# Performance work log

Hardware: AMD Instinct MI355X
Metric: run time of the kernel (lower is better)

Reference implementation:

```python
import jax, jax.numpy as jnp
import numpy as np

N_NODES = 50000
N_EDGES = 800000
EPS = 1e-5
NEG_SLOPE = 0.2


def _gatv2(x, src, dst, Wl, bl, Wr, br, att, bias, concat, N):
    # PyG GATv2Conv: xl = lin_l(x) (source side), xr = lin_r(x) (target side)
    H, C = att.shape
    xl = (x @ Wl + bl).reshape(N, H, C)
    xr = (x @ Wr + br).reshape(N, H, C)
    # per-edge message: leaky_relu(xl[j] + xr[i]), attention logit = <att, .>
    z = xl[src] + xr[dst]                      # [E, H, C]
    z = jnp.where(z > 0, z, NEG_SLOPE * z)
    logits = jnp.einsum('ehc,hc->eh', z, att)  # [E, H]
    # segment softmax over incoming edges of each target node
    m = jax.lax.stop_gradient(jax.ops.segment_max(logits, dst, num_segments=N))
    p = jnp.exp(logits - m[dst])
    s = jax.ops.segment_sum(p, dst, num_segments=N)
    alpha = p / s[dst]                         # [E, H]
    out = jax.ops.segment_sum(xl[src] * alpha[..., None], dst, num_segments=N)  # [N, H, C]
    out = out.reshape(N, H * C) if concat else out.mean(axis=1)
    return out + bias


def _bn(x, g, b):
    mu = x.mean(axis=0)
    v = x.var(axis=0)
    return (x - mu) * jax.lax.rsqrt(v + EPS) * g + b


def setup_inputs() -> dict:
    key = jax.random.key(0)
    ks = jax.random.split(key, 16)
    x = jax.random.normal(ks[0], (N_NODES, 2), jnp.float32)
    edge_index = jax.random.randint(ks[1], (2, N_EDGES), 0, N_NODES, dtype=jnp.int64)

    def lin(k, i, o):
        return jax.random.normal(k, (i, o), jnp.float32) * (1.0 / np.sqrt(i))

    inp = {'x': x, 'edge_index': edge_index}
    # layer 1: in=2, heads=8, out=16, concat
    inp['W1l'] = lin(ks[2], 2, 128); inp['b1l'] = jnp.zeros((128,), jnp.float32)
    inp['W1r'] = lin(ks[3], 2, 128); inp['b1r'] = jnp.zeros((128,), jnp.float32)
    inp['a1'] = jax.random.normal(ks[4], (8, 16), jnp.float32) * 0.1
    inp['bias1'] = jnp.zeros((128,), jnp.float32)
    inp['g1'] = jnp.ones((128,), jnp.float32); inp['be1'] = jnp.zeros((128,), jnp.float32)
    # layer 2: in=128, heads=4, out=16, concat
    inp['W2l'] = lin(ks[5], 128, 64); inp['b2l'] = jnp.zeros((64,), jnp.float32)
    inp['W2r'] = lin(ks[6], 128, 64); inp['b2r'] = jnp.zeros((64,), jnp.float32)
    inp['a2'] = jax.random.normal(ks[7], (4, 16), jnp.float32) * 0.1
    inp['bias2'] = jnp.zeros((64,), jnp.float32)
    inp['g2'] = jnp.ones((64,), jnp.float32); inp['be2'] = jnp.zeros((64,), jnp.float32)
    # layer 3: in=64, heads=1, out=2, mean (concat=False)
    inp['W3l'] = lin(ks[8], 64, 2); inp['b3l'] = jnp.zeros((2,), jnp.float32)
    inp['W3r'] = lin(ks[9], 64, 2); inp['b3r'] = jnp.zeros((2,), jnp.float32)
    inp['a3'] = jax.random.normal(ks[10], (1, 2), jnp.float32) * 0.1
    inp['bias3'] = jnp.zeros((2,), jnp.float32)
    return inp


def reference(x, edge_index, W1l, b1l, W1r, b1r, a1, bias1, g1, be1,
              W2l, b2l, W2r, b2r, a2, bias2, g2, be2,
              W3l, b3l, W3r, b3r, a3, bias3):
    N = x.shape[0]
    loops = jnp.arange(N, dtype=edge_index.dtype)
    src = jnp.concatenate([edge_index[0], loops])  # add self loops (PyG default)
    dst = jnp.concatenate([edge_index[1], loops])
    h = _gatv2(x, src, dst, W1l, b1l, W1r, b1r, a1, bias1, True, N)
    h = jax.nn.elu(_bn(h, g1, be1))  # dropout is identity in eval
    h = _gatv2(h, src, dst, W2l, b2l, W2r, b2r, a2, bias2, True, N)
    h = jax.nn.elu(_bn(h, g2, be2))
    return _gatv2(h, src, dst, W3l, b3l, W3r, b3r, a3, bias3, False, N)
```

## Files before the change

### kernel.cpp

```cpp
#include <hip/hip_runtime.h>
#include <hip/hip_bf16.h>

#define N_NODES 50000
#define N_E0    800000
#define N_ET    850000
#define EPSBN   1e-5f
#define LOG2E   1.4426950408889634f

#define LEAKY(z) fmaxf((z), 0.2f * (z))

#define OFF_C 0
#define OFF_A (128*N_NODES)
#define OFF_B (192*N_NODES)
#define OFF_STATS (256*N_NODES)
#define OFF_S1R (OFF_STATS + 512)
#define OFF_S2R (OFF_S1R + 16384)
#define OFF_P (OFF_S2R + 8192)
#define N_PARAM_TOT 118312
#define OFF_ROWPTR (OFF_P + N_PARAM_TOT)
#define OFF_DEG    (OFF_ROWPTR + 50001)
#define OFF_CURSOR (OFF_DEG + 50000)
#define OFF_BSUM   (OFF_CURSOR + 50000)
#define OFF_COL    (OFF_BSUM + 256)
#define OFF_FLAGS  (OFF_COL + 850064)
#define OFF_SCNT   (OFF_FLAGS + 2)

#define BK_CAP 131072
#define BK_CHUNK 2048

__device__ __forceinline__ float bf2f(unsigned short u) {
    return __uint_as_float(((unsigned int)u) << 16);
}
__device__ __forceinline__ unsigned short f2bf(float f) {
    unsigned int u = __float_as_uint(f);
    u += 0x7FFFu + ((u >> 16) & 1u);
    return (unsigned short)(u >> 16);
}

__global__ void prep_kernel(const unsigned short* xr, const int* ei, int* flags,
                            int* deg, float* stats, float* s1r, float* s2r, int* scnt) {
    int i = blockIdx.x * 256 + threadIdx.x;
    if (i < N_NODES) deg[i] = 0;
    if (i < 512) stats[i] = 0.f;
    if (i < 16384) s1r[i] = 0.f;
    if (i < 8192)  s2r[i] = 0.f;
    if (i < 8) scnt[i] = 0;
    if (blockIdx.x == 0) {
        __shared__ int c1, c2;
        if (threadIdx.x == 0) { c1 = 0; c2 = 0; }
        __syncthreads();
        int t = threadIdx.x;
        int l1 = 0, l2 = 0;
        for (int k = t; k < 2048; k += 256) {
            float v = bf2f(xr[k]);
            if (!(fabsf(v) <= 100.0f)) l1++;
            if (ei[2 * k + 1] != 0) l2++;
        }
        atomicAdd(&c1, l1);
        atomicAdd(&c2, l2);
        __syncthreads();
        if (t == 0) {
            flags[0] = (c1 > 16) ? 1 : 0;
            flags[1] = (c2 == 0) ? 1 : 0;
        }
    }
}

struct ParamPtrs { const void* p[23]; };

__global__ void convert_kernel(ParamPtrs ps, float* dst, const int* flags) {
    const int sizes[23] = {100000, 256,128,256,128,128,128,128,128,
                           8192,64,8192,64,64,64,64,64,
                           128,2,128,2,2,2};
    int g = blockIdx.x * 256 + threadIdx.x;
    if (g >= N_PARAM_TOT) return;
    int t = 0, off = g;
    while (off >= sizes[t]) { off -= sizes[t]; t++; }
    float v;
    if (flags[0]) v = ((const float*)ps.p[t])[off];
    else          v = bf2f(((const unsigned short*)ps.p[t])[off]);
    if (t == 5 || t == 13 || t == 21) v *= LOG2E;
    dst[g] = v;
}

__global__ void bucket_kernel(const int* ei, const int* flags, int* scnt,
                              int* dstb, int* srcb) {
    __shared__ int lcnt[8];
    __shared__ int lbase[8];
    int tid = threadIdx.x;
    if (tid < 8) lcnt[tid] = 0;
    __syncthreads();
    int base_e = blockIdx.x * BK_CHUNK;
    int i64 = flags[1];
    int src[8], dst[8], pos[8];
    #pragma unroll
    for (int u = 0; u < 8; u++) {
        int e = base_e + u * 256 + tid;
        if (e < N_ET) {
            int s, d;
            if (e < N_E0) {
                d = i64 ? ei[2 * (N_E0 + e)] : ei[N_E0 + e];
                s = i64 ? ei[2 * e] : ei[e];
            } else { s = d = e - N_E0; }
            src[u] = s; dst[u] = d;
            pos[u] = atomicAdd(&lcnt[d / 6250], 1);
        } else dst[u] = -1;
    }
    __syncthreads();
    if (tid < 8) lbase[tid] = atomicAdd(&scnt[tid], lcnt[tid]);
    __syncthreads();
    #pragma unroll
    for (int u = 0; u < 8; u++) {
        if (dst[u] >= 0) {
            int st = dst[u] / 6250;
            int gp = st * BK_CAP + lbase[st] + pos[u];
            dstb[gp] = dst[u];
            srcb[gp] = src[u];
        }
    }
}

__global__ void hist2_kernel(const int* scnt, const int* dstb, int* deg) {
    int stripe = blockIdx.x & 7;
    int bi = blockIdx.x >> 3;
    int cnt = scnt[stripe];
    const int* db = dstb + stripe * BK_CAP;
    for (int t = bi * 256 + threadIdx.x; t < cnt; t += 32 * 256)
        atomicAdd(&deg[db[t]], 1);
}

__global__ void scan1_kernel(const int* deg, int* row_ptr, int* bsum) {
    __shared__ int sh[256];
    int i = blockIdx.x * 256 + threadIdx.x;
    int v = (i < N_NODES) ? deg[i] : 0;
    sh[threadIdx.x] = v;
    __syncthreads();
    for (int off = 1; off < 256; off <<= 1) {
        int t = (threadIdx.x >= off) ? sh[threadIdx.x - off] : 0;
        __syncthreads();
        sh[threadIdx.x] += t;
        __syncthreads();
    }
    if (i < N_NODES) row_ptr[i] = sh[threadIdx.x] - v;
    if (threadIdx.x == 255) bsum[blockIdx.x] = sh[255];
}

__global__ void scan23_kernel(int* row_ptr, int* cursor, const int* bsum) {
    __shared__ int sh[256];
    int t = threadIdx.x;
    int v = (t < 196) ? bsum[t] : 0;
    sh[t] = v;
    __syncthreads();
    for (int off = 1; off < 256; off <<= 1) {
        int u = (t >= off) ? sh[t - off] : 0;
        __syncthreads();
        sh[t] += u;
        __syncthreads();
    }
    int prefix = (blockIdx.x == 0) ? 0 : sh[blockIdx.x - 1];
    int i = blockIdx.x * 256 + t;
    if (i < N_NODES) {
        int r = row_ptr[i] + prefix;
        row_ptr[i] = r;
        cursor[i] = r;
    }
    if (i == 0) row_ptr[N_NODES] = N_ET;
}

__global__ void scatter2_kernel(const int* scnt, const int* dstb, const int* srcb,
                                int* cursor, int* col) {
    int stripe = blockIdx.x & 7;
    int bi = blockIdx.x >> 3;
    int cnt = scnt[stripe];
    int off = stripe * BK_CAP;
    for (int t = bi * 256 + threadIdx.x; t < cnt; t += 32 * 256) {
        int d = dstb[off + t];
        int pos = atomicAdd(&cursor[d], 1);
        col[pos] = srcb[off + t];
    }
}

__global__ void __launch_bounds__(256) gather1_kernel(
    const int* row_ptr, const int* col, const float* x,
    const float* W1l, const float* b1l, const float* W1r, const float* b1r,
    const float* att, const float* bias, unsigned int* Cb, float* s1r)
{
    int gid = blockIdx.x * 256 + threadIdx.x;
    int n = gid >> 6;
    int lane = threadIdx.x & 63;
    float2 wl0 = *(const float2*)(W1l + 2 * lane);
    float2 wl1 = *(const float2*)(W1l + 128 + 2 * lane);
    float2 bl  = *(const float2*)(b1l + 2 * lane);
    float2 wr0 = *(const float2*)(W1r + 2 * lane);
    float2 wr1 = *(const float2*)(W1r + 128 + 2 * lane);
    float2 br  = *(const float2*)(b1r + 2 * lane);
    float2 at  = *(const float2*)(att + 2 * lane);
    float2 xd  = *(const float2*)(x + 2 * n);
    float xr0 = fmaf(xd.x, wr0.x, fmaf(xd.y, wr1.x, br.x));
    float xr1 = fmaf(xd.x, wr0.y, fmaf(xd.y, wr1.y, br.y));
    int base = __builtin_amdgcn_readfirstlane(row_ptr[n]);
    int deg  = __builtin_amdgcn_readfirstlane(row_ptr[n + 1]) - base;
    float acc0 = 0.f, acc1 = 0.f, den = 0.f;
    for (int j0 = 0; j0 < deg; j0 += 64) {
        int cnt = deg - j0; if (cnt > 64) cnt = 64;
        int msrc = col[base + j0 + lane];
        int j = 0;
        for (; j + 8 <= cnt; j += 8) {
            int s[8];
            #pragma unroll
            for (int u = 0; u < 8; u++) s[u] = __builtin_amdgcn_readlane(msrc, j + u);
            float2 xs[8];
            #pragma unroll
            for (int u = 0; u < 8; u++) xs[u] = *(const float2*)(x + 2 * s[u]);
            float xl0[8], xl1[8], part[8];
            #pragma unroll
            for (int u = 0; u < 8; u++) {
                xl0[u] = fmaf(xs[u].x, wl0.x, fmaf(xs[u].y, wl1.x, bl.x));
                xl1[u] = fmaf(xs[u].x, wl0.y, fmaf(xs[u].y, wl1.y, bl.y));
                float z0 = LEAKY(xl0[u] + xr0);
                float z1 = LEAKY(xl1[u] + xr1);
                part[u] = fmaf(z0, at.x, z1 * at.y);
            }
            #pragma unroll
            for (int m = 1; m <= 4; m <<= 1) {
                #pragma unroll
                for (int u = 0; u < 8; u++) part[u] += __shfl_xor(part[u], m, 64);
            }
            #pragma unroll
            for (int u = 0; u < 8; u++) {
                float p = exp2f(part[u]);
                acc0 = fmaf(p, xl0[u], acc0);
                acc1 = fmaf(p, xl1[u], acc1);
                den += p;
            }
        }
        for (; j < cnt; ++j) {
            int s0 = __builtin_amdgcn_readlane(msrc, j);
            float2 xs = *(const float2*)(x + 2 * s0);
            float xl0s = fmaf(xs.x, wl0.x, fmaf(xs.y, wl1.x, bl.x));
            float xl1s = fmaf(xs.x, wl0.y, fmaf(xs.y, wl1.y, bl.y));
            float z0 = LEAKY(xl0s + xr0);
            float z1 = LEAKY(xl1s + xr1);
            float part = fmaf(z0, at.x, z1 * at.y);
            part += __shfl_xor(part, 1, 64);
            part += __shfl_xor(part, 2, 64);
            part += __shfl_xor(part, 4, 64);
            float p = exp2f(part);
            acc0 = fmaf(p, xl0s, acc0);
            acc1 = fmaf(p, xl1s, acc1);
            den += p;
        }
    }
    float inv = 1.f / den;
    float2 bi = *(const float2*)(bias + 2 * lane);
    float2 outv;
    outv.x = fmaf(acc0, inv, bi.x);
    outv.y = fmaf(acc1, inv, bi.y);
    Cb[n * 64 + lane] = ((unsigned int)f2bf(outv.y) << 16) | f2bf(outv.x);
    __shared__ float sred[4][128];
    __shared__ float qred[4][128];
    int wv = threadIdx.x >> 6;
    sred[wv][2 * lane]     = outv.x;
    sred[wv][2 * lane + 1] = outv.y;
    qred[wv][2 * lane]     = outv.x * outv.x;
    qred[wv][2 * lane + 1] = outv.y * outv.y;
    __syncthreads();
    int t = threadIdx.x;
    float a;
    if (t < 128) a = sred[0][t] + sred[1][t] + sred[2][t] + sred[3][t];
    else { int c = t - 128; a = qred[0][c] + qred[1][c] + qred[2][c] + qred[3][c]; }
    atomicAdd(&s1r[(blockIdx.x & 63) * 256 + t], a);
}

__global__ void red1_kernel(const float* s1r, float* stats) {
    int t = threadIdx.x;
    int r0 = blockIdx.x * 8;
    float a = 0.f;
    #pragma unroll
    for (int r = 0; r < 8; r++) a += s1r[(r0 + r) * 256 + t];
    atomicAdd(&stats[t], a);
}

__global__ void __launch_bounds__(256) lin2_kernel(
    const unsigned int* Cb, const float* stats, const float* g1, const float* be1,
    const float* Wl, const float* bl, const float* Wr, const float* br,
    unsigned short* xl2b, float* xr2)
{
    __shared__ float h[64 * 132];
    int tid = threadIdx.x;
    int nb = blockIdx.x * 64;
    for (int i = tid; i < 64 * 64; i += 256) {
        int ni = i >> 6, kp = i & 63;
        int n = nb + ni;
        int k = 2 * kp;
        float v0 = 0.f, v1 = 0.f;
        if (n < N_NODES) {
            unsigned int pk = Cb[n * 64 + kp];
            float val0 = __uint_as_float(pk << 16);
            float val1 = __uint_as_float(pk & 0xffff0000u);
            float mu0 = stats[k] * (1.0f / N_NODES);
            float var0 = stats[128 + k] * (1.0f / N_NODES) - mu0 * mu0;
            float sc0 = g1[k] * rsqrtf(var0 + EPSBN);
            float b0 = (val0 - mu0) * sc0 + be1[k];
            v0 = b0 > 0.f ? b0 : __expf(b0) - 1.f;
            float mu1 = stats[k + 1] * (1.0f / N_NODES);
            float var1 = stats[128 + k + 1] * (1.0f / N_NODES) - mu1 * mu1;
            float sc1 = g1[k + 1] * rsqrtf(var1 + EPSBN);
            float b1 = (val1 - mu1) * sc1 + be1[k + 1];
            v1 = b1 > 0.f ? b1 : __expf(b1) - 1.f;
        }
        h[ni * 132 + k]     = v0;
        h[ni * 132 + k + 1] = v1;
    }
    __syncthreads();
    int kt = (tid & 15) * 4;
    int nt = (tid >> 4) * 4;
    float accl[4][4], accr[4][4];
    #pragma unroll
    for (int i = 0; i < 4; i++) {
        #pragma unroll
        for (int k = 0; k < 4; k++) { accl[i][k] = 0.f; accr[i][k] = 0.f; }
    }
    for (int j = 0; j < 128; j += 4) {
        float4 hv[4];
        #pragma unroll
        for (int i = 0; i < 4; i++)
            hv[i] = *(const float4*)&h[(nt + i) * 132 + j];
        #pragma unroll
        for (int jj = 0; jj < 4; jj++) {
            float4 wl4 = *(const float4*)&Wl[(j + jj) * 64 + kt];
            float4 wr4 = *(const float4*)&Wr[(j + jj) * 64 + kt];
            #pragma unroll
            for (int i = 0; i < 4; i++) {
                float hvv = (jj == 0) ? hv[i].x : (jj == 1) ? hv[i].y :
                            (jj == 2) ? hv[i].z : hv[i].w;
                accl[i][0] += hvv * wl4.x; accl[i][1] += hvv * wl4.y;
                accl[i][2] += hvv * wl4.z; accl[i][3] += hvv * wl4.w;
                accr[i][0] += hvv * wr4.x; accr[i][1] += hvv * wr4.y;
                accr[i][2] += hvv * wr4.z; accr[i][3] += hvv * wr4.w;
            }
        }
    }
    float4 blv = *(const float4*)&bl[kt];
    float4 brv = *(const float4*)&br[kt];
    #pragma unroll
    for (int i = 0; i < 4; i++) {
        int n = nb + nt + i;
        if (n < N_NODES) {
            ushort4 ob;
            ob.x = f2bf(accl[i][0] + blv.x);
            ob.y = f2bf(accl[i][1] + blv.y);
            ob.z = f2bf(accl[i][2] + blv.z);
            ob.w = f2bf(accl[i][3] + blv.w);
            *(ushort4*)&xl2b[n * 64 + kt] = ob;
            float4 o;
            o.x = accr[i][0] + brv.x; o.y = accr[i][1] + brv.y;
            o.z = accr[i][2] + brv.z; o.w = accr[i][3] + brv.w;
            *(float4*)&xr2[n * 64 + kt] = o;
        }
    }
}

__global__ void __launch_bounds__(256) gather2_kernel(
    const int* row_ptr, const int* col, const unsigned short* xl2b, const float* xr2,
    const float* att, const float* bias, float* C, float* s2r)
{
    int gid = blockIdx.x * 256 + threadIdx.x;
    int n = gid >> 6;
    int lane = threadIdx.x & 63;
    int grp = lane >> 4;
    int cidx = lane & 15;
    float4 xrv = *(const float4*)(xr2 + n * 64 + 4 * cidx);
    float4 atv = *(const float4*)(att + 4 * cidx);
    int base = __builtin_amdgcn_readfirstlane(row_ptr[n]);
    int deg  = __builtin_amdgcn_readfirstlane(row_ptr[n + 1]) - base;
    float4 acc = make_float4(0.f, 0.f, 0.f, 0.f);
    float den = 0.f;
    for (int j0 = 0; j0 < deg; j0 += 64) {
        int cnt = deg - j0; if (cnt > 64) cnt = 64;
        int msrc = col[base + j0 + lane];
        for (int j4 = 0; j4 < cnt; j4 += 8) {
            int e0 = j4 + grp, e1 = j4 + 4 + grp;
            int s0 = __shfl(msrc, e0, 64);
            int s1 = __shfl(msrc, e1, 64);
            bool v0 = e0 < cnt, v1 = e1 < cnt;
            s0 = v0 ? s0 : 0;
            s1 = v1 ? s1 : 0;
            uint2 ba = *(const uint2*)(xl2b + (size_t)s0 * 64 + 4 * cidx);
            uint2 bb = *(const uint2*)(xl2b + (size_t)s1 * 64 + 4 * cidx);
            float a0 = __uint_as_float(ba.x << 16);
            float a1 = __uint_as_float(ba.x & 0xffff0000u);
            float a2 = __uint_as_float(ba.y << 16);
            float a3 = __uint_as_float(ba.y & 0xffff0000u);
            float b0 = __uint_as_float(bb.x << 16);
            float b1 = __uint_as_float(bb.x & 0xffff0000u);
            float b2 = __uint_as_float(bb.y << 16);
            float b3 = __uint_as_float(bb.y & 0xffff0000u);
            float pa = LEAKY(a0 + xrv.x) * atv.x;
            pa = fmaf(LEAKY(a1 + xrv.y), atv.y, pa);
            pa = fmaf(LEAKY(a2 + xrv.z), atv.z, pa);
            pa = fmaf(LEAKY(a3 + xrv.w), atv.w, pa);
            float pb = LEAKY(b0 + xrv.x) * atv.x;
            pb = fmaf(LEAKY(b1 + xrv.y), atv.y, pb);
            pb = fmaf(LEAKY(b2 + xrv.z), atv.z, pb);
            pb = fmaf(LEAKY(b3 + xrv.w), atv.w, pb);
            pa += __shfl_xor(pa, 1, 64);
            pa += __shfl_xor(pa, 2, 64);
            pb += __shfl_xor(pb, 1, 64);
            pb += __shfl_xor(pb, 2, 64);
            float ea = v0 ? exp2f(pa) : 0.f;
            float eb = v1 ? exp2f(pb) : 0.f;
            acc.x = fmaf(ea, a0, acc.x); acc.x = fmaf(eb, b0, acc.x);
            acc.y = fmaf(ea, a1, acc.y); acc.y = fmaf(eb, b1, acc.y);
            acc.z = fmaf(ea, a2, acc.z); acc.z = fmaf(eb, b2, acc.z);
            acc.w = fmaf(ea, a3, acc.w); acc.w = fmaf(eb, b3, acc.w);
            den += ea + eb;
        }
    }
    acc.x += __shfl_xor(acc.x, 16, 64); acc.x += __shfl_xor(acc.x, 32, 64);
    acc.y += __shfl_xor(acc.y, 16, 64); acc.y += __shfl_xor(acc.y, 32, 64);
    acc.z += __shfl_xor(acc.z, 16, 64); acc.z += __shfl_xor(acc.z, 32, 64);
    acc.w += __shfl_xor(acc.w, 16, 64); acc.w += __shfl_xor(acc.w, 32, 64);
    den += __shfl_xor(den, 16, 64);
    den += __shfl_xor(den, 32, 64);
    float inv = 1.f / den;
    float4 bi = *(const float4*)(bias + 4 * cidx);
    float4 o;
    o.x = fmaf(acc.x, inv, bi.x);
    o.y = fmaf(acc.y, inv, bi.y);
    o.z = fmaf(acc.z, inv, bi.z);
    o.w = fmaf(acc.w, inv, bi.w);
    if (lane < 16) *(float4*)(C + n * 64 + 4 * cidx) = o;
    __shared__ float sred[4][64];
    __shared__ float qred[4][64];
    int wv = threadIdx.x >> 6;
    if (lane < 16) {
        int c = 4 * cidx;
        sred[wv][c]     = o.x; qred[wv][c]     = o.x * o.x;
        sred[wv][c + 1] = o.y; qred[wv][c + 1] = o.y * o.y;
        sred[wv][c + 2] = o.z; qred[wv][c + 2] = o.z * o.z;
        sred[wv][c + 3] = o.w; qred[wv][c + 3] = o.w * o.w;
    }
    __syncthreads();
    int t = threadIdx.x;
    if (t < 128) {
        float a;
        if (t < 64) a = sred[0][t] + sred[1][t] + sred[2][t] + sred[3][t];
        else { int c = t - 64; a = qred[0][c] + qred[1][c] + qred[2][c] + qred[3][c]; }
        atomicAdd(&s2r[(blockIdx.x & 63) * 128 + t], a);
    }
}

__global__ void red2_kernel(const float* s2r, float* stats) {
    int t = threadIdx.x;
    int r0 = blockIdx.x * 8;
    float a = 0.f;
    #pragma unroll
    for (int r = 0; r < 8; r++) a += s2r[(r0 + r) * 128 + t];
    atomicAdd(&stats[t], a);
}

__global__ void __launch_bounds__(256) lin3_kernel(
    const float* C, const float* stats2, const float* g2, const float* be2,
    const float* Wl, const float* bl, const float* Wr, const float* br,
    float* xl3, float* xr3)
{
    int gid = blockIdx.x * 256 + threadIdx.x;
    int n = gid >> 6;
    int lane = threadIdx.x & 63;
    if (n >= N_NODES) return;
    float mu = stats2[lane] * (1.0f / N_NODES);
    float var = stats2[64 + lane] * (1.0f / N_NODES) - mu * mu;
    float sc = g2[lane] * rsqrtf(var + EPSBN);
    float of = be2[lane] - mu * sc;
    float v = C[n * 64 + lane] * sc + of;
    float h = v > 0.f ? v : __expf(v) - 1.f;
    float2 wlv = *(const float2*)(Wl + 2 * lane);
    float2 wrv = *(const float2*)(Wr + 2 * lane);
    float a0 = h * wlv.x, a1 = h * wlv.y;
    float r0 = h * wrv.x, r1 = h * wrv.y;
    #pragma unroll
    for (int m = 1; m < 64; m <<= 1) {
        a0 += __shfl_xor(a0, m, 64);
        a1 += __shfl_xor(a1, m, 64);
        r0 += __shfl_xor(r0, m, 64);
        r1 += __shfl_xor(r1, m, 64);
    }
    if (lane == 0) {
        xl3[2 * n]     = a0 + bl[0];
        xl3[2 * n + 1] = a1 + bl[1];
        xr3[2 * n]     = r0 + br[0];
        xr3[2 * n + 1] = r1 + br[1];
    }
}

__global__ void __launch_bounds__(256) gather3_kernel(
    const int* row_ptr, const int* col,
    const float* xl3, const float* xr3,
    const float* att, const float* bias,
    void* out, const int* flags) {
    int gid = blockIdx.x * 256 + threadIdx.x;
    int n = gid >> 2;
    int q = threadIdx.x & 3;
    if (n >= N_NODES) return;
    float a0 = att[0], a1 = att[1];
    float xr0 = xr3[2 * n], xr1 = xr3[2 * n + 1];
    float acc0 = 0.f, acc1 = 0.f, den = 0.f;
    int e0 = row_ptr[n], e1 = row_ptr[n + 1];
    for (int e = e0 + q; e < e1; e += 4) {
        int src = col[e];
        float2 xs = *(const float2*)(xl3 + 2 * src);
        float z0 = LEAKY(xs.x + xr0);
        float z1 = LEAKY(xs.y + xr1);
        float p = exp2f(fmaf(z0, a0, z1 * a1));
        acc0 = fmaf(p, xs.x, acc0);
        acc1 = fmaf(p, xs.y, acc1);
        den += p;
    }
    acc0 += __shfl_xor(acc0, 1, 64); acc0 += __shfl_xor(acc0, 2, 64);
    acc1 += __shfl_xor(acc1, 1, 64); acc1 += __shfl_xor(acc1, 2, 64);
    den  += __shfl_xor(den, 1, 64);  den  += __shfl_xor(den, 2, 64);
    if (q == 0) {
        float inv = 1.f / den;
        float v0 = fmaf(acc0, inv, bias[0]);
        float v1 = fmaf(acc1, inv, bias[1]);
        if (flags[0]) {
            ((float*)out)[2 * n] = v0;
            ((float*)out)[2 * n + 1] = v1;
        } else {
            ((__hip_bfloat16*)out)[2 * n] = __float2bfloat16(v0);
            ((__hip_bfloat16*)out)[2 * n + 1] = __float2bfloat16(v1);
        }
    }
}

extern "C" void kernel_launch(void* const* d_in, const int* in_sizes, int n_in,
                              void* d_out, int out_size, void* d_ws, size_t ws_size,
                              hipStream_t stream) {
    float* W = (float*)d_ws;
    float* C = W + OFF_C;
    float* A = W + OFF_A;
    float* B = W + OFF_B;
    float* STATS = W + OFF_STATS;
    float* S1R = W + OFF_S1R;
    float* S2R = W + OFF_S2R;
    float* P = W + OFF_P;
    int* ROWPTR = (int*)(W + OFF_ROWPTR);
    int* DEG    = (int*)(W + OFF_DEG);
    int* CURSOR = (int*)(W + OFF_CURSOR);
    int* BSUM   = (int*)(W + OFF_BSUM);
    int* COL    = (int*)(W + OFF_COL);
    int* FLAGS  = (int*)(W + OFF_FLAGS);
    int* SCNT   = (int*)(W + OFF_SCNT);
    int* DSTB   = (int*)(W + OFF_C);
    int* SRCB   = DSTB + 8 * BK_CAP;

    const int* ei = (const int*)d_in[1];

    float* Px  = P;
    float* W1l = Px + 100000; float* b1l = W1l + 256; float* W1r = b1l + 128; float* b1r = W1r + 256;
    float* a1  = b1r + 128;   float* bias1 = a1 + 128; float* g1 = bias1 + 128; float* be1 = g1 + 128;
    float* W2l = be1 + 128;   float* b2l = W2l + 8192; float* W2r = b2l + 64;  float* b2r = W2r + 8192;
    float* a2  = b2r + 64;    float* bias2 = a2 + 64;  float* g2 = bias2 + 64; float* be2 = g2 + 64;
    float* W3l = be2 + 64;    float* b3l = W3l + 128;  float* W3r = b3l + 2;   float* b3r = W3r + 128;
    float* a3  = b3r + 2;     float* bias3 = a3 + 2;

    prep_kernel<<<196, 256, 0, stream>>>((const unsigned short*)d_in[0], ei, FLAGS, DEG, STATS, S1R, S2R, SCNT);

    ParamPtrs ps;
    ps.p[0] = d_in[0];
    for (int j = 1; j < 23; j++) ps.p[j] = d_in[j + 1];
    convert_kernel<<<(N_PARAM_TOT + 255) / 256, 256, 0, stream>>>(ps, P, FLAGS);

    bucket_kernel<<<(N_ET + BK_CHUNK - 1) / BK_CHUNK, 256, 0, stream>>>(ei, FLAGS, SCNT, DSTB, SRCB);
    hist2_kernel<<<256, 256, 0, stream>>>(SCNT, DSTB, DEG);
    scan1_kernel<<<196, 256, 0, stream>>>(DEG, ROWPTR, BSUM);
    scan23_kernel<<<196, 256, 0, stream>>>(ROWPTR, CURSOR, BSUM);
    scatter2_kernel<<<256, 256, 0, stream>>>(SCNT, DSTB, SRCB, CURSOR, COL);

    gather1_kernel<<<N_NODES * 64 / 256, 256, 0, stream>>>(ROWPTR, COL, Px, W1l, b1l, W1r, b1r, a1, bias1, (unsigned int*)C, S1R);
    red1_kernel<<<8, 256, 0, stream>>>(S1R, STATS);

    lin2_kernel<<<(N_NODES + 63) / 64, 256, 0, stream>>>((const unsigned int*)C, STATS, g1, be1, W2l, b2l, W2r, b2r, (unsigned short*)A, B);
    gather2_kernel<<<N_NODES * 64 / 256, 256, 0, stream>>>(ROWPTR, COL, (const unsigned short*)A, B, a2, bias2, C, S2R);
    red2_kernel<<<8, 128, 0, stream>>>(S2R, STATS + 256);

    lin3_kernel<<<N_NODES * 64 / 256, 256, 0, stream>>>(C, STATS + 256, g2, be2, W3l, b3l, W3r, b3r, A, B);
    gather3_kernel<<<(N_NODES * 4 + 255) / 256, 256, 0, stream>>>(ROWPTR, COL, A, B, a3, bias3, d_out, FLAGS);
}
```

Baseline: 338.9 us.

## Split layer-1 gather wavefront into two half-waves processing alternate edges

The layer-1 GATv2 gather kernel now has each lane handle 4 channels instead of 2. The two 32-lane halves of a wavefront process alternate edges in parallel and are combined with a cross-half shuffle at the end. This halves the serial edge iterations per node and shortens the per-edge head reduction from three shuffles to two. In exchange each lane does twice the arithmetic per edge, padded edges are masked with a valid predicate, and an extra final reduction is added.

```diff
diff --git a/kernel.cpp b/kernel.cpp
--- a/kernel.cpp
+++ b/kernel.cpp
@@ -188,82 +188,84 @@
     int gid = blockIdx.x * 256 + threadIdx.x;
     int n = gid >> 6;
     int lane = threadIdx.x & 63;
-    float2 wl0 = *(const float2*)(W1l + 2 * lane);
-    float2 wl1 = *(const float2*)(W1l + 128 + 2 * lane);
-    float2 bl  = *(const float2*)(b1l + 2 * lane);
-    float2 wr0 = *(const float2*)(W1r + 2 * lane);
-    float2 wr1 = *(const float2*)(W1r + 128 + 2 * lane);
-    float2 br  = *(const float2*)(b1r + 2 * lane);
-    float2 at  = *(const float2*)(att + 2 * lane);
+    int g = lane >> 5;
+    int cl = lane & 31;
+    int cb = cl * 4;
+    float4 wl0 = *(const float4*)(W1l + cb);
+    float4 wl1 = *(const float4*)(W1l + 128 + cb);
+    float4 blv = *(const float4*)(b1l + cb);
+    float4 atv = *(const float4*)(att + cb);
     float2 xd  = *(const float2*)(x + 2 * n);
-    float xr0 = fmaf(xd.x, wr0.x, fmaf(xd.y, wr1.x, br.x));
-    float xr1 = fmaf(xd.x, wr0.y, fmaf(xd.y, wr1.y, br.y));
+    float4 wr0 = *(const float4*)(W1r + cb);
+    float4 wr1 = *(const float4*)(W1r + 128 + cb);
+    float4 brv = *(const float4*)(b1r + cb);
+    float4 xrk;
+    xrk.x = fmaf(xd.x, wr0.x, fmaf(xd.y, wr1.x, brv.x));
+    xrk.y = fmaf(xd.x, wr0.y, fmaf(xd.y, wr1.y, brv.y));
+    xrk.z = fmaf(xd.x, wr0.z, fmaf(xd.y, wr1.z, brv.z));
+    xrk.w = fmaf(xd.x, wr0.w, fmaf(xd.y, wr1.w, brv.w));
     int base = __builtin_amdgcn_readfirstlane(row_ptr[n]);
     int deg  = __builtin_amdgcn_readfirstlane(row_ptr[n + 1]) - base;
-    float acc0 = 0.f, acc1 = 0.f, den = 0.f;
+    float4 acc = make_float4(0.f, 0.f, 0.f, 0.f);
+    float den = 0.f;
     for (int j0 = 0; j0 < deg; j0 += 64) {
         int cnt = deg - j0; if (cnt > 64) cnt = 64;
         int msrc = col[base + j0 + lane];
-        int j = 0;
-        for (; j + 8 <= cnt; j += 8) {
-            int s[8];
+        for (int j2 = 0; j2 < cnt; j2 += 8) {
             #pragma unroll
-            for (int u = 0; u < 8; u++) s[u] = __builtin_amdgcn_readlane(msrc, j + u);
-            float2 xs[8];
-            #pragma unroll
-            for (int u = 0; u < 8; u++) xs[u] = *(const float2*)(x + 2 * s[u]);
-            float xl0[8], xl1[8], part[8];
-            #pragma unroll
-            for (int u = 0; u < 8; u++) {
-                xl0[u] = fmaf(xs[u].x, wl0.x, fmaf(xs[u].y, wl1.x, bl.x));
-                xl1[u] = fmaf(xs[u].x, wl0.y, fmaf(xs[u].y, wl1.y, bl.y));
-                float z0 = LEAKY(xl0[u] + xr0);
-                float z1 = LEAKY(xl1[u] + xr1);
-                part[u] = fmaf(z0, at.x, z1 * at.y);
-            }
-            #pragma unroll
-            for (int m = 1; m <= 4; m <<= 1) {
-                #pragma unroll
-                for (int u = 0; u < 8; u++) part[u] += __shfl_xor(part[u], m, 64);
-            }
-            #pragma unroll
-            for (int u = 0; u < 8; u++) {
-                float p = exp2f(part[u]);
-                acc0 = fmaf(p, xl0[u], acc0);
-                acc1 = fmaf(p, xl1[u], acc1);
+            for (int u = 0; u < 4; u++) {
+                int e = j2 + 2 * u + g;
+                int s = __shfl(msrc, e, 64);
+                bool valid = e < cnt;
+                s = valid ? s : 0;
+                float2 xs = *(const float2*)(x + 2 * s);
+                float4 xl;
+                xl.x = fmaf(xs.x, wl0.x, fmaf(xs.y, wl1.x, blv.x));
+                xl.y = fmaf(xs.x, wl0.y, fmaf(xs.y, wl1.y, blv.y));
+                xl.z = fmaf(xs.x, wl0.z, fmaf(xs.y, wl1.z, blv.z));
+                xl.w = fmaf(xs.x, wl0.w, fmaf(xs.y, wl1.w, blv.w));
+                float part = LEAKY(xl.x + xrk.x) * atv.x;
+                part = fmaf(LEAKY(xl.y + xrk.y), atv.y, part);
+                part = fmaf(LEAKY(xl.z + xrk.z), atv.z, part);
+                part = fmaf(LEAKY(xl.w + xrk.w), atv.w, part);
+                part += __shfl_xor(part, 1, 64);
+                part += __shfl_xor(part, 2, 64);
+                float p = valid ? exp2f(part) : 0.f;
+                acc.x = fmaf(p, xl.x, acc.x);
+                acc.y = fmaf(p, xl.y, acc.y);
+                acc.z = fmaf(p, xl.z, acc.z);
+                acc.w = fmaf(p, xl.w, acc.w);
                 den += p;
             }
         }
-        for (; j < cnt; ++j) {
-            int s0 = __builtin_amdgcn_readlane(msrc, j);
-            float2 xs = *(const float2*)(x + 2 * s0);
-            float xl0s = fmaf(xs.x, wl0.x, fmaf(xs.y, wl1.x, bl.x));
-            float xl1s = fmaf(xs.x, wl0.y, fmaf(xs.y, wl1.y, bl.y));
-            float z0 = LEAKY(xl0s + xr0);
-            float z1 = LEAKY(xl1s + xr1);
-            float part = fmaf(z0, at.x, z1 * at.y);
-            part += __shfl_xor(part, 1, 64);
-            part += __shfl_xor(part, 2, 64);
-            part += __shfl_xor(part, 4, 64);
-            float p = exp2f(part);
-            acc0 = fmaf(p, xl0s, acc0);
-            acc1 = fmaf(p, xl1s, acc1);
-            den += p;
-        }
-    }
+    }
+    acc.x += __shfl_xor(acc.x, 32, 64);
+    acc.y += __shfl_xor(acc.y, 32, 64);
+    acc.z += __shfl_xor(acc.z, 32, 64);
+    acc.w += __shfl_xor(acc.w, 32, 64);
+    den += __shfl_xor(den, 32, 64);
     float inv = 1.f / den;
-    float2 bi = *(const float2*)(bias + 2 * lane);
-    float2 outv;
-    outv.x = fmaf(acc0, inv, bi.x);
-    outv.y = fmaf(acc1, inv, bi.y);
-    Cb[n * 64 + lane] = ((unsigned int)f2bf(outv.y) << 16) | f2bf(outv.x);
+    float4 bi = *(const float4*)(bias + cb);
+    float4 o;
+    o.x = fmaf(acc.x, inv, bi.x);
+    o.y = fmaf(acc.y, inv, bi.y);
+    o.z = fmaf(acc.z, inv, bi.z);
+    o.w = fmaf(acc.w, inv, bi.w);
+    if (g == 0) {
+        uint2 pk;
+        pk.x = ((unsigned int)f2bf(o.y) << 16) | f2bf(o.x);
+        pk.y = ((unsigned int)f2bf(o.w) << 16) | f2bf(o.z);
+        *(uint2*)(Cb + n * 64 + 2 * cl) = pk;
+    }
     __shared__ float sred[4][128];
     __shared__ float qred[4][128];
     int wv = threadIdx.x >> 6;
-    sred[wv][2 * lane]     = outv.x;
-    sred[wv][2 * lane + 1] = outv.y;
-    qred[wv][2 * lane]     = outv.x * outv.x;
-    qred[wv][2 * lane + 1] = outv.y * outv.y;
+    if (g == 0) {
+        sred[wv][cb]     = o.x; qred[wv][cb]     = o.x * o.x;
+        sred[wv][cb + 1] = o.y; qred[wv][cb + 1] = o.y * o.y;
+        sred[wv][cb + 2] = o.z; qred[wv][cb + 2] = o.z * o.z;
+        sred[wv][cb + 3] = o.w; qred[wv][cb + 3] = o.w * o.w;
+    }
     __syncthreads();
     int t = threadIdx.x;
     float a;
```

Measured after the change: 340.2 us. Within noise of the previous version (+0.4%).
